# Kernel optimization log

Measured on AMD Instinct MI355X. Metric: run time of the kernel, lower is better.

## Reference

```python
import jax, jax.numpy as jnp
import numpy as np

N_NODES = 100000
N_EDGES = 1600000
IN_F = 256
OUT_F = 128


def setup_inputs() -> dict:
    key = jax.random.key(0)
    k1, k2, k3, k4, k5 = jax.random.split(key, 5)
    x = jax.random.normal(k1, (N_NODES, IN_F), dtype=jnp.float32)
    edge_rows = jax.random.randint(k2, (N_EDGES,), 0, N_NODES, dtype=jnp.int32)
    edge_cols = jax.random.randint(k3, (N_EDGES,), 0, N_NODES, dtype=jnp.int32)
    edge_vals = jax.random.uniform(k4, (N_EDGES,), dtype=jnp.float32)
    # glorot init for weight, zeros for bias (matches reset_parameters)
    limit = float(np.sqrt(6.0 / (IN_F + OUT_F)))
    weight = jax.random.uniform(k5, (IN_F, OUT_F), dtype=jnp.float32,
                                minval=-limit, maxval=limit)
    bias = jnp.zeros((OUT_F,), dtype=jnp.float32)
    return {"x": x, "edge_rows": edge_rows, "edge_cols": edge_cols,
            "edge_vals": edge_vals, "weight": weight, "bias": bias}


def reference(x, edge_rows, edge_cols, edge_vals, weight, bias):
    # dense projection: [N, in] @ [in, out] -> [N, out]
    h = x @ weight
    # spmm(adj, h): out[r] = sum_{edges e with row r} vals[e] * h[col[e]]
    msgs = edge_vals[:, None] * h[edge_cols]          # [E, out]
    agg = jax.ops.segment_sum(msgs, edge_rows, num_segments=N_NODES)
    return agg + bias
```

## Files before the change

kernel.cpp:

```cpp
#include <hip/hip_runtime.h>


typedef __attribute__((ext_vector_type(8))) short short8;
typedef __attribute__((ext_vector_type(4))) float floatx4;
typedef __attribute__((ext_vector_type(2))) int intv2;

#define WT_K 264
#define GM_NODES 128
#define BSHIFT 6
#define BROWS 64
#define CAP 1280
#define NBMAX 1600
#define EPB 6400
#define CSH 4
#define OVFCAP 65536

static __device__ __forceinline__ uint f2bf(float x) {
  uint u = __float_as_uint(x);
  return (u + 0x7fffu + ((u >> 16) & 1u)) >> 16;
}

union u4s8 { uint4 u; short8 s; };

__global__ __launch_bounds__(256) void conv_w(const float* __restrict__ w,
                                              ushort* __restrict__ wt,
                                              int* __restrict__ cursors,
                                              int n_ints) {
  const int f = blockIdx.x;
  const int k = threadIdx.x;
  wt[f * WT_K + k] = (ushort)f2bf(w[k * 128 + f]);
  for (int i = blockIdx.x * 256 + threadIdx.x; i < n_ints; i += 128 * 256)
    cursors[i] = 0;
}

__global__ __launch_bounds__(256) void gemm_mfma(const float* __restrict__ x,
                                                 const ushort* __restrict__ wt,
                                                 ushort* __restrict__ h,
                                                 int n_nodes) {
  __shared__ ushort lw[128 * WT_K];
  const int t = threadIdx.x;
  const int lane = t & 63;
  const int wq = t >> 6;
  const int quad = lane >> 4;
  const int l15 = lane & 15;
  const int row0 = blockIdx.x * GM_NODES;

  {
    const uint4* src = (const uint4*)wt;
    uint4* dst = (uint4*)lw;
    for (int i = t; i < (128 * WT_K * 2) / 16; i += 256) dst[i] = src[i];
  }

  floatx4 acc[2][8];
#pragma unroll
  for (int nt = 0; nt < 2; ++nt)
#pragma unroll
    for (int mt = 0; mt < 8; ++mt) acc[nt][mt] = (floatx4){0.f, 0.f, 0.f, 0.f};

  const int n0 = row0 + wq * 32 + l15;
  const int n1 = n0 + 16;
  const bool v0 = (n0 < n_nodes), v1 = (n1 < n_nodes);
  const float* p0 = x + (size_t)(v0 ? n0 : 0) * 256 + quad * 8;
  const float* p1 = x + (size_t)(v1 ? n1 : 0) * 256 + quad * 8;
  const float4 z4 = make_float4(0.f, 0.f, 0.f, 0.f);

  float4 cா[4];
  float4 cur0a = v0 ? *(const float4*)(p0 + 0) : z4;
  float4 cur0b = v0 ? *(const float4*)(p0 + 4) : z4;
  float4 cur1a = v1 ? *(const float4*)(p1 + 0) : z4;
  float4 cur1b = v1 ? *(const float4*)(p1 + 4) : z4;
  (void)cா;

  __syncthreads();

  for (int kc = 0; kc < 8; ++kc) {
    float4 nxt0a, nxt0b, nxt1a, nxt1b;
    if (kc < 7) {
      const int o = (kc + 1) * 32;
      nxt0a = v0 ? *(const float4*)(p0 + o + 0) : z4;
      nxt0b = v0 ? *(const float4*)(p0 + o + 4) : z4;
      nxt1a = v1 ? *(const float4*)(p1 + o + 0) : z4;
      nxt1b = v1 ? *(const float4*)(p1 + o + 4) : z4;
    }

    u4s8 bf0, bf1;
    bf0.u.x = f2bf(cur0a.x) | (f2bf(cur0a.y) << 16);
    bf0.u.y = f2bf(cur0a.z) | (f2bf(cur0a.w) << 16);
    bf0.u.z = f2bf(cur0b.x) | (f2bf(cur0b.y) << 16);
    bf0.u.w = f2bf(cur0b.z) | (f2bf(cur0b.w) << 16);
    bf1.u.x = f2bf(cur1a.x) | (f2bf(cur1a.y) << 16);
    bf1.u.y = f2bf(cur1a.z) | (f2bf(cur1a.w) << 16);
    bf1.u.z = f2bf(cur1b.x) | (f2bf(cur1b.y) << 16);
    bf1.u.w = f2bf(cur1b.z) | (f2bf(cur1b.w) << 16);

#pragma unroll
    for (int mt = 0; mt < 8; ++mt) {
      const short8 afr =
          *(const short8*)&lw[(mt * 16 + l15) * WT_K + kc * 32 + quad * 8];
      acc[0][mt] = __builtin_amdgcn_mfma_f32_16x16x32_bf16(afr, bf0.s,
                                                           acc[0][mt], 0, 0, 0);
      acc[1][mt] = __builtin_amdgcn_mfma_f32_16x16x32_bf16(afr, bf1.s,
                                                           acc[1][mt], 0, 0, 0);
    }
    cur0a = nxt0a; cur0b = nxt0b; cur1a = nxt1a; cur1b = nxt1b;
  }

#pragma unroll
  for (int nt = 0; nt < 2; ++nt) {
    const int node = row0 + wq * 32 + nt * 16 + l15;
    if (node < n_nodes) {
#pragma unroll
      for (int mt = 0; mt < 8; ++mt) {
        uint2 p;
        p.x = f2bf(acc[nt][mt][0]) | (f2bf(acc[nt][mt][1]) << 16);
        p.y = f2bf(acc[nt][mt][2]) | (f2bf(acc[nt][mt][3]) << 16);
        *(uint2*)&h[(size_t)node * 128 + mt * 16 + quad * 4] = p;
      }
    }
  }
}

__global__ __launch_bounds__(256) void fill_bin(
    const int* __restrict__ erows, const int* __restrict__ ecols,
    const float* __restrict__ evals, int* __restrict__ cursors,
    int2* __restrict__ bcv, int* __restrict__ ovf_cnt,
    int4* __restrict__ ovf, int n_edges, int nb) {
  __shared__ int2 rec[EPB];
  __shared__ short bkt[EPB];
  __shared__ int cnt[NBMAX], bas[NBMAX], cur[NBMAX];
  const int t = threadIdx.x;
  const int e0 = blockIdx.x * EPB;
  const int n = min(EPB, n_edges - e0);
  if (n <= 0) return;

  for (int b = t; b < nb; b += 256) { cnt[b] = 0; cur[b] = 0; }
  __syncthreads();

  {
    int i = t;
    for (; i + 768 < n; i += 1024) {
      int r0 = __builtin_nontemporal_load(&erows[e0 + i]);
      int r1 = __builtin_nontemporal_load(&erows[e0 + i + 256]);
      int r2 = __builtin_nontemporal_load(&erows[e0 + i + 512]);
      int r3 = __builtin_nontemporal_load(&erows[e0 + i + 768]);
      int c0 = __builtin_nontemporal_load(&ecols[e0 + i]);
      int c1 = __builtin_nontemporal_load(&ecols[e0 + i + 256]);
      int c2 = __builtin_nontemporal_load(&ecols[e0 + i + 512]);
      int c3 = __builtin_nontemporal_load(&ecols[e0 + i + 768]);
      float v0 = __builtin_nontemporal_load(&evals[e0 + i]);
      float v1 = __builtin_nontemporal_load(&evals[e0 + i + 256]);
      float v2 = __builtin_nontemporal_load(&evals[e0 + i + 512]);
      float v3 = __builtin_nontemporal_load(&evals[e0 + i + 768]);
      int2 p0; p0.x = c0 | ((r0 & (BROWS - 1)) << 17); p0.y = __float_as_int(v0);
      int2 p1; p1.x = c1 | ((r1 & (BROWS - 1)) << 17); p1.y = __float_as_int(v1);
      int2 p2; p2.x = c2 | ((r2 & (BROWS - 1)) << 17); p2.y = __float_as_int(v2);
      int2 p3; p3.x = c3 | ((r3 & (BROWS - 1)) << 17); p3.y = __float_as_int(v3);
      rec[i] = p0; rec[i + 256] = p1; rec[i + 512] = p2; rec[i + 768] = p3;
      const int b0 = r0 >> BSHIFT, b1 = r1 >> BSHIFT;
      const int b2 = r2 >> BSHIFT, b3 = r3 >> BSHIFT;
      bkt[i] = (short)b0; bkt[i + 256] = (short)b1;
      bkt[i + 512] = (short)b2; bkt[i + 768] = (short)b3;
      atomicAdd(&cnt[b0], 1); atomicAdd(&cnt[b1], 1);
      atomicAdd(&cnt[b2], 1); atomicAdd(&cnt[b3], 1);
    }
    for (; i < n; i += 256) {
      const int r = __builtin_nontemporal_load(&erows[e0 + i]);
      const int c = __builtin_nontemporal_load(&ecols[e0 + i]);
      const float v = __builtin_nontemporal_load(&evals[e0 + i]);
      int2 p; p.x = c | ((r & (BROWS - 1)) << 17); p.y = __float_as_int(v);
      rec[i] = p;
      const int b = r >> BSHIFT;
      bkt[i] = (short)b;
      atomicAdd(&cnt[b], 1);
    }
  }
  __syncthreads();

  for (int b = t; b < nb; b += 256) {
    const int c = cnt[b];
    if (c > 0) bas[b] = atomicAdd(&cursors[b << CSH], c);
  }
  __syncthreads();

  for (int i = t; i < n; i += 256) {
    const int b = (int)bkt[i];
    const int loc = atomicAdd(&cur[b], 1);
    const int pos = bas[b] + loc;
    const int2 p = rec[i];
    if (pos < CAP) {
      bcv[(size_t)b * CAP + pos] = p;
    } else {
      int op = atomicAdd(ovf_cnt, 1);
      if (op < OVFCAP) {
        int4 q;
        q.x = (b << BSHIFT) | ((p.x >> 17) & (BROWS - 1));
        q.y = p.x & 0x1FFFF;
        q.z = p.y; q.w = 0;
        ovf[op] = q;
      }
    }
  }
}

__global__ __launch_bounds__(256) void sort_gather(
    const ushort* __restrict__ h, const int* __restrict__ cursors,
    const int2* __restrict__ bcv, const float* __restrict__ bias,
    float* __restrict__ out, int n_nodes, int nb) {
  __shared__ int2 buf[CAP];
  __shared__ int cnt[BROWS], start[BROWS], cur[BROWS];
  const int b = blockIdx.x;
  const int t = threadIdx.x;
  const int nrec = min(cursors[b << CSH], CAP);
  if (t < BROWS) cnt[t] = 0;
  __syncthreads();

  const int2* src = &bcv[(size_t)b * CAP];
  int2 r[5];
#pragma unroll
  for (int j = 0; j < 5; ++j) {
    const int i = t + j * 256;
    if (i < nrec) {
      intv2 rv = __builtin_nontemporal_load((const intv2*)&src[i]);
      r[j].x = rv[0]; r[j].y = rv[1];
    } else {
      r[j].x = 0; r[j].y = 0;
    }
  }
#pragma unroll
  for (int j = 0; j < 5; ++j) {
    const int i = t + j * 256;
    if (i < nrec) atomicAdd(&cnt[((uint)r[j].x) >> 17], 1);
  }
  __syncthreads();

  if (t < BROWS) {
    int c = cnt[t];
    int s = c;
#pragma unroll
    for (int off = 1; off < 64; off <<= 1) {
      int u = __shfl_up(s, off, 64);
      if (t >= off) s += u;
    }
    start[t] = s - c;
    cur[t] = s - c;
  }
  __syncthreads();

#pragma unroll
  for (int j = 0; j < 5; ++j) {
    const int i = t + j * 256;
    if (i < nrec) {
      int pos = atomicAdd(&cur[((uint)r[j].x) >> 17], 1);
      buf[pos] = r[j];
    }
  }
  __syncthreads();

  const int lane = t & 63;
  const int w = t >> 6;
  const float2 bv = ((const float2*)bias)[lane];
  for (int rr = w * 16; rr < w * 16 + 16; ++rr) {
    const int node = b * BROWS + rr;
    if (node >= n_nodes) break;
    float2 acca = bv;
    float2 accb = make_float2(0.f, 0.f);
    int p = start[rr];
    const int p1 = start[rr] + cnt[rr];
    for (; p + 8 <= p1; p += 8) {
      int2 e0 = buf[p + 0];
      int2 e1 = buf[p + 1];
      int2 e2 = buf[p + 2];
      int2 e3 = buf[p + 3];
      int2 e4 = buf[p + 4];
      int2 e5 = buf[p + 5];
      int2 e6 = buf[p + 6];
      int2 e7 = buf[p + 7];
      uint u0 = ((const uint*)(h + (size_t)(e0.x & 0x1FFFF) * 128))[lane];
      uint u1 = ((const uint*)(h + (size_t)(e1.x & 0x1FFFF) * 128))[lane];
      uint u2 = ((const uint*)(h + (size_t)(e2.x & 0x1FFFF) * 128))[lane];
      uint u3 = ((const uint*)(h + (size_t)(e3.x & 0x1FFFF) * 128))[lane];
      uint u4 = ((const uint*)(h + (size_t)(e4.x & 0x1FFFF) * 128))[lane];
      uint u5 = ((const uint*)(h + (size_t)(e5.x & 0x1FFFF) * 128))[lane];
      uint u6 = ((const uint*)(h + (size_t)(e6.x & 0x1FFFF) * 128))[lane];
      uint u7 = ((const uint*)(h + (size_t)(e7.x & 0x1FFFF) * 128))[lane];
      float v0 = __int_as_float(e0.y), v1 = __int_as_float(e1.y);
      float v2 = __int_as_float(e2.y), v3 = __int_as_float(e3.y);
      float v4 = __int_as_float(e4.y), v5 = __int_as_float(e5.y);
      float v6 = __int_as_float(e6.y), v7 = __int_as_float(e7.y);
      acca.x += v0 * __uint_as_float(u0 << 16);
      acca.y += v0 * __uint_as_float(u0 & 0xffff0000u);
      accb.x += v1 * __uint_as_float(u1 << 16);
      accb.y += v1 * __uint_as_float(u1 & 0xffff0000u);
      acca.x += v2 * __uint_as_float(u2 << 16);
      acca.y += v2 * __uint_as_float(u2 & 0xffff0000u);
      accb.x += v3 * __uint_as_float(u3 << 16);
      accb.y += v3 * __uint_as_float(u3 & 0xffff0000u);
      acca.x += v4 * __uint_as_float(u4 << 16);
      acca.y += v4 * __uint_as_float(u4 & 0xffff0000u);
      accb.x += v5 * __uint_as_float(u5 << 16);
      accb.y += v5 * __uint_as_float(u5 & 0xffff0000u);
      acca.x += v6 * __uint_as_float(u6 << 16);
      acca.y += v6 * __uint_as_float(u6 & 0xffff0000u);
      accb.x += v7 * __uint_as_float(u7 << 16);
      accb.y += v7 * __uint_as_float(u7 & 0xffff0000u);
    }
    for (; p < p1; ++p) {
      int2 ev = buf[p];
      float v = __int_as_float(ev.y);
      uint u = ((const uint*)(h + (size_t)(ev.x & 0x1FFFF) * 128))[lane];
      acca.x += v * __uint_as_float(u << 16);
      acca.y += v * __uint_as_float(u & 0xffff0000u);
    }
    float2 accf;
    accf.x = acca.x + accb.x;
    accf.y = acca.y + accb.y;
    ((float2*)(out + (size_t)node * 128))[lane] = accf;
  }
}

__global__ __launch_bounds__(256) void ovf_scatter(
    const ushort* __restrict__ h, const int* __restrict__ ovf_cnt,
    const int4* __restrict__ ovf, float* __restrict__ out) {
  const int n = min(*ovf_cnt, OVFCAP);
  const int lane = threadIdx.x & 63;
  const int wid = (blockIdx.x * 256 + threadIdx.x) >> 6;
  const int nw = gridDim.x * 4;
  for (int e = wid; e < n; e += nw) {
    int4 recq = ovf[e];
    float v = __int_as_float(recq.z);
    uint u = ((const uint*)(h + (size_t)recq.y * 128))[lane];
    float* op = out + (size_t)recq.x * 128 + lane * 2;
    atomicAdd(op, v * __uint_as_float(u << 16));
    atomicAdd(op + 1, v * __uint_as_float(u & 0xffff0000u));
  }
}

__global__ __launch_bounds__(256) void init_bias(float* __restrict__ out,
                                                 const float* __restrict__ bias,
                                                 int n4) {
  int i = blockIdx.x * 256 + threadIdx.x;
  if (i < n4) {
    float4 b = ((const float4*)bias)[i & 31];
    ((float4*)out)[i] = b;
  }
}

__global__ __launch_bounds__(256) void scatter_edges(
    const ushort* __restrict__ h, const int* __restrict__ erows,
    const int* __restrict__ ecols, const float* __restrict__ evals,
    float* __restrict__ out, int n_edges) {
  int e = blockIdx.x * 4 + (threadIdx.x >> 6);
  if (e >= n_edges) return;
  int lane = threadIdx.x & 63;
  int row = erows[e];
  int col = ecols[e];
  float v = evals[e];
  uint u = ((const uint*)(h + (size_t)col * 128))[lane];
  float* op = out + (size_t)row * 128 + lane * 2;
  atomicAdd(op, v * __uint_as_float(u << 16));
  atomicAdd(op + 1, v * __uint_as_float(u & 0xffff0000u));
}

extern "C" void kernel_launch(void* const* d_in, const int* in_sizes, int n_in,
                              void* d_out, int out_size, void* d_ws, size_t ws_size,
                              hipStream_t stream) {
  const float* x     = (const float*)d_in[0];
  const int*   erows = (const int*)d_in[1];
  const int*   ecols = (const int*)d_in[2];
  const float* evals = (const float*)d_in[3];
  const float* w     = (const float*)d_in[4];
  const float* bias  = (const float*)d_in[5];
  float* out = (float*)d_out;

  const int n_nodes = in_sizes[0] / 256;
  const int n_edges = in_sizes[1];
  const int nb_buckets = (n_nodes + BROWS - 1) >> BSHIFT;

  char* ws = (char*)d_ws;
  size_t off = 0;
  ushort* h  = (ushort*)(ws + off);  off += ((size_t)n_nodes * 128 * 2 + 255) & ~255ull;
  ushort* wt = (ushort*)(ws + off);  off += ((size_t)128 * WT_K * 2 + 255) & ~255ull;
  const size_t cur_ints = (((size_t)nb_buckets) << CSH) + 16;
  int* cursors = (int*)(ws + off);   off += (cur_ints * 4 + 255) & ~255ull;
  int2* bcv    = (int2*)(ws + off);  off += ((size_t)nb_buckets * CAP * 8 + 255) & ~255ull;
  int4* ovf    = (int4*)(ws + off);  off += (size_t)OVFCAP * 16;
  const bool bucket_ok = (off <= ws_size) && (nb_buckets <= NBMAX) &&
                         (n_nodes <= 102400);
  int* ovf_cnt = cursors + (((size_t)nb_buckets) << CSH);

  const int zero_ints = bucket_ok ? (int)cur_ints : 0;
  conv_w<<<128, 256, 0, stream>>>(w, wt, cursors, zero_ints);
  const int gemm_blocks = (n_nodes + GM_NODES - 1) / GM_NODES;
  gemm_mfma<<<gemm_blocks, 256, 0, stream>>>(x, wt, h, n_nodes);

  if (bucket_ok) {
    const int eblocks = (n_edges + EPB - 1) / EPB;
    fill_bin<<<eblocks, 256, 0, stream>>>(erows, ecols, evals, cursors, bcv,
                                          ovf_cnt, ovf, n_edges, nb_buckets);
    sort_gather<<<nb_buckets, 256, 0, stream>>>(h, cursors, bcv, bias, out,
                                                n_nodes, nb_buckets);
    ovf_scatter<<<32, 256, 0, stream>>>(h, ovf_cnt, ovf, out);
  } else {
    const int n4 = out_size / 4;
    init_bias<<<(n4 + 255) / 256, 256, 0, stream>>>(out, bias, n4);
    scatter_edges<<<(n_edges + 3) / 4, 256, 0, stream>>>(h, erows, ecols, evals,
                                                         out, n_edges);
  }
}
```

Baseline: 299.4 us.

## Fuse GEMM and edge binning into one launch with interleaved block roles

```diff
diff --git a/kernel.cpp b/kernel.cpp
--- a/kernel.cpp
+++ b/kernel.cpp
@@ -11,9 +11,10 @@
 #define BROWS 64
 #define CAP 1280
 #define NBMAX 1600
-#define EPB 6400
+#define EPB 4800
 #define CSH 4
 #define OVFCAP 65536
+#define SMEM_BYTES 67584
 
 static __device__ __forceinline__ uint f2bf(float x) {
   uint u = __float_as_uint(x);
@@ -33,17 +34,15 @@
     cursors[i] = 0;
 }
 
-__global__ __launch_bounds__(256) void gemm_mfma(const float* __restrict__ x,
-                                                 const ushort* __restrict__ wt,
-                                                 ushort* __restrict__ h,
-                                                 int n_nodes) {
-  __shared__ ushort lw[128 * WT_K];
+static __device__ __forceinline__ void gemm_body(
+    const float* __restrict__ x, const ushort* __restrict__ wt,
+    ushort* __restrict__ h, int n_nodes, int row0, char* smem) {
+  ushort* lw = (ushort*)smem;
   const int t = threadIdx.x;
   const int lane = t & 63;
   const int wq = t >> 6;
   const int quad = lane >> 4;
   const int l15 = lane & 15;
-  const int row0 = blockIdx.x * GM_NODES;
 
   {
     const uint4* src = (const uint4*)wt;
@@ -64,12 +63,10 @@
   const float* p1 = x + (size_t)(v1 ? n1 : 0) * 256 + quad * 8;
   const float4 z4 = make_float4(0.f, 0.f, 0.f, 0.f);
 
-  float4 cா[4];
   float4 cur0a = v0 ? *(const float4*)(p0 + 0) : z4;
   float4 cur0b = v0 ? *(const float4*)(p0 + 4) : z4;
   float4 cur1a = v1 ? *(const float4*)(p1 + 0) : z4;
   float4 cur1b = v1 ? *(const float4*)(p1 + 4) : z4;
-  (void)cா;
 
   __syncthreads();
 
@@ -120,16 +117,17 @@
   }
 }
 
-__global__ __launch_bounds__(256) void fill_bin(
+static __device__ __forceinline__ void fill_body(
     const int* __restrict__ erows, const int* __restrict__ ecols,
     const float* __restrict__ evals, int* __restrict__ cursors,
     int2* __restrict__ bcv, int* __restrict__ ovf_cnt,
-    int4* __restrict__ ovf, int n_edges, int nb) {
-  __shared__ int2 rec[EPB];
-  __shared__ short bkt[EPB];
-  __shared__ int cnt[NBMAX], bas[NBMAX], cur[NBMAX];
+    int4* __restrict__ ovf, int n_edges, int nb, int e0, char* smem) {
+  int2* rec = (int2*)smem;
+  short* bkt = (short*)(smem + EPB * 8);
+  int* cnt = (int*)(smem + EPB * 10);
+  int* bas = cnt + NBMAX;
+  int* cur = bas + NBMAX;
   const int t = threadIdx.x;
-  const int e0 = blockIdx.x * EPB;
   const int n = min(EPB, n_edges - e0);
   if (n <= 0) return;
 
@@ -200,6 +198,41 @@
       }
     }
   }
+}
+
+__global__ __launch_bounds__(256) void gemm_fill(
+    const float* __restrict__ x, const ushort* __restrict__ wt,
+    ushort* __restrict__ h, const int* __restrict__ erows,
+    const int* __restrict__ ecols, const float* __restrict__ evals,
+    int* __restrict__ cursors, int2* __restrict__ bcv,
+    int* __restrict__ ovf_cnt, int4* __restrict__ ovf,
+    int n_nodes, int n_edges, int nb, int nfill) {
+  __shared__ __align__(16) char smem[SMEM_BYTES];
+  const int bid = blockIdx.x;
+  const int total = gridDim.x;
+  const int nf2 = nfill * 2;
+  int role, rid;
+  if (nf2 <= total) {
+    if (bid < nf2) { role = bid & 1; rid = bid >> 1; }
+    else           { role = 0;       rid = bid - nfill; }
+  } else {
+    role = (bid < nfill) ? 1 : 0;
+    rid = role ? bid : bid - nfill;
+  }
+  if (role == 0) {
+    gemm_body(x, wt, h, n_nodes, rid * GM_NODES, smem);
+  } else {
+    fill_body(erows, ecols, evals, cursors, bcv, ovf_cnt, ovf, n_edges, nb,
+              rid * EPB, smem);
+  }
+}
+
+__global__ __launch_bounds__(256) void gemm_mfma(const float* __restrict__ x,
+                                                 const ushort* __restrict__ wt,
+                                                 ushort* __restrict__ h,
+                                                 int n_nodes) {
+  __shared__ __align__(16) char smem[SMEM_BYTES];
+  gemm_body(x, wt, h, n_nodes, blockIdx.x * GM_NODES, smem);
 }
 
 __global__ __launch_bounds__(256) void sort_gather(
@@ -390,17 +423,19 @@
 
   const int zero_ints = bucket_ok ? (int)cur_ints : 0;
   conv_w<<<128, 256, 0, stream>>>(w, wt, cursors, zero_ints);
-  const int gemm_blocks = (n_nodes + GM_NODES - 1) / GM_NODES;
-  gemm_mfma<<<gemm_blocks, 256, 0, stream>>>(x, wt, h, n_nodes);
 
   if (bucket_ok) {
-    const int eblocks = (n_edges + EPB - 1) / EPB;
-    fill_bin<<<eblocks, 256, 0, stream>>>(erows, ecols, evals, cursors, bcv,
-                                          ovf_cnt, ovf, n_edges, nb_buckets);
+    const int ngemm = (n_nodes + GM_NODES - 1) / GM_NODES;
+    const int nfill = (n_edges + EPB - 1) / EPB;
+    gemm_fill<<<ngemm + nfill, 256, 0, stream>>>(
+        x, wt, h, erows, ecols, evals, cursors, bcv, ovf_cnt, ovf,
+        n_nodes, n_edges, nb_buckets, nfill);
     sort_gather<<<nb_buckets, 256, 0, stream>>>(h, cursors, bcv, bias, out,
                                                 n_nodes, nb_buckets);
     ovf_scatter<<<32, 256, 0, stream>>>(h, ovf_cnt, ovf, out);
   } else {
+    const int gemm_blocks = (n_nodes + GM_NODES - 1) / GM_NODES;
+    gemm_mfma<<<gemm_blocks, 256, 0, stream>>>(x, wt, h, n_nodes);
     const int n4 = out_size / 4;
     init_bias<<<(n4 + 255) / 256, 256, 0, stream>>>(out, bias, n4);
     scatter_edges<<<(n_edges + 3) / 4, 256, 0, stream>>>(h, erows, ecols, evals,
```

New measurement: 293.2 us. 1.02x faster.
